# Kernel optimization log

Measured on AMD Instinct MI355X. Metric: run time of the kernel, lower is better.

## Reference

```python
import jax, jax.numpy as jnp
import numpy as np

B, S, H, NH = 2, 2048, 2048, 16
HD = H // NH


def setup_inputs() -> dict:
    key = jax.random.key(0)
    ks = jax.random.split(key, 10)
    s = 1.0 / np.sqrt(H)
    x = jax.random.normal(ks[0], (B, S, H), dtype=jnp.float32)
    # additive causal mask: 0 on/below diagonal, -1e9 above
    causal = jnp.tril(jnp.ones((S, S), dtype=bool))
    mask = jnp.where(causal, 0.0, -1e9).astype(jnp.float32)[None, None]
    return {
        "x": x,
        "mask": mask,
        "wq": jax.random.normal(ks[1], (H, H), jnp.float32) * s,
        "bq": jnp.zeros((H,), jnp.float32),
        "wk": jax.random.normal(ks[2], (H, H), jnp.float32) * s,
        "bk": jnp.zeros((H,), jnp.float32),
        "wv": jax.random.normal(ks[3], (H, H), jnp.float32) * s,
        "bv": jnp.zeros((H,), jnp.float32),
        "wo": jax.random.normal(ks[4], (H, H), jnp.float32) * s,
        "bo": jnp.zeros((H,), jnp.float32),
    }


def reference(x, mask, wq, bq, wk, bk, wv, bv, wo, bo):
    b, s, _ = x.shape
    scale = HD ** (-0.5)
    # projections -> [b, nh, s, hd]
    def split_heads(t):
        return t.reshape(b, s, NH, HD).transpose(0, 2, 1, 3)
    q = split_heads(x @ wq + bq)
    k = split_heads(x @ wk + bk)
    v = split_heads(x @ wv + bv)
    scores = jnp.einsum('bhqd,bhkd->bhqk', q, k) * scale + mask
    attn = jax.nn.softmax(scores, axis=-1)
    out = jnp.einsum('bhqk,bhkd->bhqd', attn, v)
    out = out.transpose(0, 2, 1, 3).reshape(b, s, H)
    return out @ wo + bo
```

## Files before the change

kernel.cpp:

```cpp
#include <hip/hip_runtime.h>


using bf16x8 = __attribute__((ext_vector_type(8))) short;
using bf16x4 = __attribute__((ext_vector_type(4))) short;
using f32x4  = __attribute__((ext_vector_type(4))) float;

#define S_LEN 2048
#define NHEAD 16
#define HDIM  128
#define HID   2048

__device__ __forceinline__ unsigned short f2bf(float f) {
    unsigned int u = __float_as_uint(f);
    u += 0x7fffu + ((u >> 16) & 1u);
    return (unsigned short)(u >> 16);
}
__device__ __forceinline__ void gl2lds16(const void* g, void* l) {
    __builtin_amdgcn_global_load_lds(
        (const __attribute__((address_space(1))) void*)g,
        (__attribute__((address_space(3))) void*)l, 16, 0, 0);
}

__device__ __forceinline__ f32x4 pv_mfma(bf16x4 a, bf16x4 b, f32x4 c) {
#if defined(__HIP_DEVICE_COMPILE__)
#if __has_builtin(__builtin_amdgcn_mfma_f32_16x16x16bf16_1k)
    return __builtin_amdgcn_mfma_f32_16x16x16bf16_1k(a, b, c, 0, 0, 0);
#else
    asm("v_mfma_f32_16x16x16_bf16 %0, %1, %2, %0" : "+v"(c) : "v"(a), "v"(b));
    return c;
#endif
#else
    (void)a; (void)b;
    return c;
#endif
}

__global__ void convert_x(const float* __restrict__ x, unsigned short* __restrict__ xb) {
    int i = (blockIdx.x * 256 + threadIdx.x) * 4;
    float4 v = *(const float4*)(x + i);
    ushort4 o;
    o.x = f2bf(v.x); o.y = f2bf(v.y); o.z = f2bf(v.z); o.w = f2bf(v.w);
    *(ushort4*)(xb + i) = o;
}

__global__ void convert_wt(const float* __restrict__ w0, const float* __restrict__ w1,
                           const float* __restrict__ w2, const float* __restrict__ w3,
                           unsigned short* __restrict__ t0, unsigned short* __restrict__ t1,
                           unsigned short* __restrict__ t2, unsigned short* __restrict__ t3) {
    __shared__ float tile[64][65];
    int z = blockIdx.z;
    const float* src = (z == 0) ? w0 : (z == 1) ? w1 : (z == 2) ? w2 : w3;
    unsigned short* dst = (z == 0) ? t0 : (z == 1) ? t1 : (z == 2) ? t2 : t3;
    int r0 = blockIdx.y * 64, c0 = blockIdx.x * 64;
    int t = threadIdx.x;
    for (int i = t; i < 64 * 64; i += 256) {
        int r = i >> 6, c = i & 63;
        tile[r][c] = src[(size_t)(r0 + r) * HID + c0 + c];
    }
    __syncthreads();
    for (int i = t; i < 64 * 64; i += 256) {
        int r = i & 63, c = i >> 6;
        dst[(size_t)(c0 + c) * HID + r0 + r] = f2bf(tile[r][c]);
    }
}

__device__ __forceinline__ void sched0() { __builtin_amdgcn_sched_barrier(0); }
__device__ __forceinline__ void w_lgkm4() { asm volatile("s_waitcnt lgkmcnt(4)" ::: "memory"); sched0(); }
__device__ __forceinline__ void w_lgkm0() { asm volatile("s_waitcnt lgkmcnt(0)" ::: "memory"); sched0(); }
template <int NJ> __device__ __forceinline__ void w_lgkm_4nj() {
    if constexpr (NJ == 3) { asm volatile("s_waitcnt lgkmcnt(7)" ::: "memory"); }
    else                   { asm volatile("s_waitcnt lgkmcnt(6)" ::: "memory"); }
    sched0();
}
template <int NJ> __device__ __forceinline__ void w_vm_ns() {
    if constexpr (NJ == 3) { asm volatile("s_waitcnt vmcnt(7)" ::: "memory"); }
    else                   { asm volatile("s_waitcnt vmcnt(6)" ::: "memory"); }
    sched0();
}
__device__ __forceinline__ void w_vm2() { asm volatile("s_waitcnt vmcnt(2)" ::: "memory"); sched0(); }
__device__ __forceinline__ void w_vm0() { asm volatile("s_waitcnt vmcnt(0)" ::: "memory"); sched0(); }
__device__ __forceinline__ void barx() {
    asm volatile("" ::: "memory");
    __builtin_amdgcn_s_barrier();
    asm volatile("" ::: "memory");
}

template <int MODE, int NJ>
__launch_bounds__(512, 2)
__global__ void gemmT(const unsigned short* __restrict__ A,
                      const unsigned short* __restrict__ Bt0,
                      const float* __restrict__ bias0,
                      const float* __restrict__ bias1,
                      const float* __restrict__ bias2,
                      unsigned short* __restrict__ C0,
                      unsigned short* __restrict__ C1,
                      unsigned short* __restrict__ C2,
                      float* __restrict__ Cf) {
    constexpr int BN = NJ * 64;
    __shared__ __align__(16) unsigned short lds[2 * 16384 + 2 * NJ * 4096];
    unsigned short* const A0 = lds;
    unsigned short* const A1 = lds + 16384;
    unsigned short* const B0 = lds + 32768;
    unsigned short* const B1 = lds + 32768 + NJ * 4096;

    const int CPX = (MODE == 1) ? 64 : 32;
    int vb = (blockIdx.x & 7) * CPX + (blockIdx.x >> 3);
    int m0  = (vb & 15) * 256;
    int n0g = (vb >> 4) * BN;

    int tid = threadIdx.x;
    int lane = tid & 63;
    int wv_ = tid >> 6;
    int wr = wv_ >> 2, wc = wv_ & 3;
    int l15 = lane & 15, quad = lane >> 4;

    int tr = tid >> 3;
    int tc = ((tid & 7) ^ (tr & 7)) << 3;
    const unsigned short* gA = A   + (size_t)(m0  + tr) * HID + tc;
    const unsigned short* gB = Bt0 + (size_t)(n0g + tr) * HID + tc;
    const int td8 = tid * 8;

    int arow0 = (wr * 128 + l15) * 64;
    int brow0 = (wc * (16 * NJ) + l15) * 64;
    int sw0 = ((quad ^ (l15 & 7)) << 3);
    int sw1 = (((4 + quad) ^ (l15 & 7)) << 3);

    f32x4 acc[8][NJ];
#pragma unroll
    for (int i = 0; i < 8; ++i)
#pragma unroll
        for (int j = 0; j < NJ; ++j) acc[i][j] = (f32x4){0.f, 0.f, 0.f, 0.f};

    bf16x8 aX[4], aY[4], b0v[NJ], b1v[NJ];

#define STAGE(kt, AD, BD) do { int _kc = (kt) * 64;                          \
    gl2lds16(gA + _kc,             (AD) + td8);                              \
    gl2lds16(gA + 64 * HID + _kc,  (AD) + 4096 + td8);                       \
    gl2lds16(gA + 128 * HID + _kc, (AD) + 8192 + td8);                       \
    gl2lds16(gA + 192 * HID + _kc, (AD) + 12288 + td8);                      \
    _Pragma("unroll")                                                        \
    for (int _r = 0; _r < NJ; ++_r)                                          \
        gl2lds16(gB + (size_t)(_r * 64) * HID + _kc, (BD) + _r * 4096 + td8); } while (0)

#define LDA4(dst, AD, QB, SW) do {                                           \
    dst[0] = *(const bf16x8*)((AD) + arow0 + ((QB) + 0) * 1024 + (SW));      \
    dst[1] = *(const bf16x8*)((AD) + arow0 + ((QB) + 1) * 1024 + (SW));      \
    dst[2] = *(const bf16x8*)((AD) + arow0 + ((QB) + 2) * 1024 + (SW));      \
    dst[3] = *(const bf16x8*)((AD) + arow0 + ((QB) + 3) * 1024 + (SW)); } while (0)

#define LDB(dst, BD, SW) do {                                                \
    _Pragma("unroll")                                                        \
    for (int _n = 0; _n < NJ; ++_n)                                          \
        dst[_n] = *(const bf16x8*)((BD) + brow0 + _n * 1024 + (SW)); } while (0)

#define MF(Q, a, b) do {                                                     \
    __builtin_amdgcn_s_setprio(1);                                           \
    _Pragma("unroll")                                                        \
    for (int mi = 0; mi < 4; ++mi)                                           \
        _Pragma("unroll")                                                    \
        for (int nj = 0; nj < NJ; ++nj)                                      \
            acc[(Q) * 4 + mi][nj] =                                          \
                __builtin_amdgcn_mfma_f32_16x16x32_bf16(a[mi], b[nj],        \
                                                        acc[(Q) * 4 + mi][nj], 0, 0, 0); \
    __builtin_amdgcn_s_setprio(0); } while (0)

#define TILE(AD, BD, AN, BN_, ks) do {                                       \
    LDA4(aY, AD, 4, sw0);                                      \
    w_lgkm4();                                   \
    MF(0, aX, b0v);                                                          \
    LDA4(aX, AD, 0, sw1);                                                    \
    LDB(b1v, BD, sw1);                                   \
    w_lgkm_4nj<NJ>();                                          \
    MF(1, aY, b0v);                                                          \
    LDA4(aY, AD, 4, sw1);                                      \
    w_lgkm4();                                             \
    MF(0, aX, b1v);                                                          \
    w_lgkm0();                                \
    barx();                              \
    STAGE(ks, AD, BD);                          \
    w_vm_ns<NJ>();                        \
    barx();                                  \
    LDA4(aX, AN, 0, sw0);                                                    \
    LDB(b0v, BN_, sw0);                   \
    sched0();                                                                \
    MF(1, aY, b1v);                          \
} while (0)

    STAGE(0, A0, B0);
    STAGE(1, A1, B1);
    w_vm_ns<NJ>();
    barx();
    LDA4(aX, A0, 0, sw0);
    LDB(b0v, B0, sw0);

    for (int t = 0; t < 32; t += 2) {
        TILE(A0, B0, A1, B1, (t + 2 < 32) ? t + 2 : 31);
        TILE(A1, B1, A0, B0, (t + 3 < 32) ? t + 3 : 31);
    }
    asm volatile("s_waitcnt vmcnt(0) lgkmcnt(0)" ::: "memory");

#undef TILE
#undef STAGE
#undef LDA4
#undef LDB
#undef MF

#pragma unroll
    for (int j = 0; j < NJ; ++j) {
        int n = n0g + wc * (16 * NJ) + j * 16 + l15;
        int zj = (MODE == 1) ? (n >> 11) : 0;
        int nn = (MODE == 1) ? (n & 2047) : n;
        float bn = (MODE == 1)
                     ? ((zj == 0) ? bias0[nn] : (zj == 1) ? bias1[nn] : bias2[nn])
                     : bias0[nn];
        unsigned short* Cz = (zj == 0) ? C0 : (zj == 1) ? C1 : C2;
#pragma unroll
        for (int i = 0; i < 8; ++i) {
            int mb = m0 + wr * 128 + i * 16 + quad * 4;
            if (MODE == 1 && zj == 2) {
                int b = mb >> 11, s = mb & 2047, h = nn >> 7, d = nn & 127;
                int kt = s >> 4, qv = (s >> 2) & 3, ct = d >> 4, lv = d & 15;
                size_t addr = ((((size_t)((b << 4) + h) * 128 + kt) * 4 + (ct >> 1)) * 4 + qv) * 128
                              + lv * 8 + (ct & 1) * 4;
                ushort4 o;
                o.x = f2bf(acc[i][j][0] + bn);
                o.y = f2bf(acc[i][j][1] + bn);
                o.z = f2bf(acc[i][j][2] + bn);
                o.w = f2bf(acc[i][j][3] + bn);
                *(ushort4*)&Cz[addr] = o;
            } else {
#pragma unroll
                for (int reg = 0; reg < 4; ++reg) {
                    int m = mb + reg;
                    float v = acc[i][j][reg] + bn;
                    if (MODE == 0) {
                        Cf[(size_t)m * HID + nn] = v;
                    } else {
                        int b = m >> 11, s = m & 2047, h = nn >> 7, d = nn & 127;
                        if (zj == 1) {
                            int kt = s >> 4, lk = s & 15, kk = d >> 5, qk = (d >> 3) & 3, e = d & 7;
                            size_t addr = ((((size_t)((b << 4) + h) * 128 + kt) * 4 + kk) * 4 + qk) * 128
                                          + lk * 8 + e;
                            Cz[addr] = f2bf(v);
                        } else {
                            Cz[(size_t)(((b << 4) + h) * S_LEN + s) * HDIM + d] = f2bf(v);
                        }
                    }
                }
            }
        }
    }
}

__launch_bounds__(256, 2)
__global__ void attn_kernel(const unsigned short* __restrict__ Qg,
                            const unsigned short* __restrict__ Kp,
                            const unsigned short* __restrict__ Vp,
                            unsigned short* __restrict__ O) {
    __shared__ __align__(16) unsigned short kv[2][4096];

    int linear = blockIdx.x;
    int xcd = linear & 7;
    int u = linear >> 3;
    int bh = xcd * 4 + (u & 3);
    int q = u >> 2;
    int b = bh >> 4, h = bh & 15;

    int tid = threadIdx.x, lane = tid & 63, w = tid >> 6;
    int l15 = lane & 15, quad = lane >> 4;

    const unsigned short* Qb = Qg + (size_t)bh * (S_LEN * HDIM);
    const unsigned short* Kg = Kp + (size_t)bh * 262144;
    const unsigned short* Vg = Vp + (size_t)bh * 262144;
    const float k2 = 0.08838834764831845f * 1.4426950408889634f;

    const int frag = quad * 128 + l15 * 8;
    const int td8 = tid * 8;

#define VLO(x) __builtin_shufflevector(x, x, 0, 1, 2, 3)
#define VHI(x) __builtin_shufflevector(x, x, 4, 5, 6, 7)
#define ASTAGE(kt, bf) do { size_t _g = (size_t)(kt) * 2048 + td8;             \
    gl2lds16(Kg + _g, &kv[bf][td8]);                                           \
    gl2lds16(Vg + _g, &kv[bf][2048 + td8]); } while (0)

    auto run_qblock = [&](int qb) {
        int s  = 4 * qb + w;
        int r0 = s * 16;
        int N  = 4 * qb + 4;

        bf16x8 qf[4];
#pragma unroll
        for (int kk = 0; kk < 4; ++kk)
            qf[kk] = *(const bf16x8*)&Qb[(size_t)(r0 + l15) * HDIM + kk * 32 + quad * 8];

        f32x4 o_acc[8];
#pragma unroll
        for (int c = 0; c < 8; ++c) o_acc[c] = (f32x4){0.f, 0.f, 0.f, 0.f};
        float l_part = 0.f;

        ASTAGE(0, 0);
        for (int kt = 0; kt < N; ++kt) {
            int nk = (kt + 1 < N) ? kt + 1 : kt;
            ASTAGE(nk, (kt + 1) & 1);
            w_vm2();
            barx();

            const unsigned short* KL = &kv[kt & 1][frag];
            const unsigned short* VL = &kv[kt & 1][2048 + frag];
            bf16x8 kb0 = *(const bf16x8*)(KL);
            bf16x8 kb1 = *(const bf16x8*)(KL + 512);
            bf16x8 kb2 = *(const bf16x8*)(KL + 1024);
            bf16x8 kb3 = *(const bf16x8*)(KL + 1536);
            bf16x8 v0 = *(const bf16x8*)(VL);
            bf16x8 v1 = *(const bf16x8*)(VL + 512);
            bf16x8 v2 = *(const bf16x8*)(VL + 1024);
            bf16x8 v3 = *(const bf16x8*)(VL + 1536);

            f32x4 st0 = (f32x4){0.f, 0.f, 0.f, 0.f};
            f32x4 st1 = (f32x4){0.f, 0.f, 0.f, 0.f};
            __builtin_amdgcn_s_setprio(1);
            st0 = __builtin_amdgcn_mfma_f32_16x16x32_bf16(kb0, qf[0], st0, 0, 0, 0);
            st1 = __builtin_amdgcn_mfma_f32_16x16x32_bf16(kb1, qf[1], st1, 0, 0, 0);
            st0 = __builtin_amdgcn_mfma_f32_16x16x32_bf16(kb2, qf[2], st0, 0, 0, 0);
            st1 = __builtin_amdgcn_mfma_f32_16x16x32_bf16(kb3, qf[3], st1, 0, 0, 0);
            __builtin_amdgcn_s_setprio(0);
            f32x4 stv = st0 + st1;

            float p0, p1, p2, p3;
            int doff = kt - s;
            if (doff >= 0) {
                int d16 = doff << 4;
                p0 = (d16 + quad * 4 + 0 <= l15) ? exp2f(stv[0] * k2) : 0.f;
                p1 = (d16 + quad * 4 + 1 <= l15) ? exp2f(stv[1] * k2) : 0.f;
                p2 = (d16 + quad * 4 + 2 <= l15) ? exp2f(stv[2] * k2) : 0.f;
                p3 = (d16 + quad * 4 + 3 <= l15) ? exp2f(stv[3] * k2) : 0.f;
            } else {
                p0 = exp2f(stv[0] * k2); p1 = exp2f(stv[1] * k2);
                p2 = exp2f(stv[2] * k2); p3 = exp2f(stv[3] * k2);
            }
            l_part += (p0 + p1) + (p2 + p3);

            bf16x4 pf;
            pf[0] = (short)f2bf(p0); pf[1] = (short)f2bf(p1);
            pf[2] = (short)f2bf(p2); pf[3] = (short)f2bf(p3);

            __builtin_amdgcn_s_setprio(1);
            o_acc[0] = pv_mfma(pf, VLO(v0), o_acc[0]);
            o_acc[1] = pv_mfma(pf, VHI(v0), o_acc[1]);
            o_acc[2] = pv_mfma(pf, VLO(v1), o_acc[2]);
            o_acc[3] = pv_mfma(pf, VHI(v1), o_acc[3]);
            o_acc[4] = pv_mfma(pf, VLO(v2), o_acc[4]);
            o_acc[5] = pv_mfma(pf, VHI(v2), o_acc[5]);
            o_acc[6] = pv_mfma(pf, VLO(v3), o_acc[6]);
            o_acc[7] = pv_mfma(pf, VHI(v3), o_acc[7]);
            __builtin_amdgcn_s_setprio(0);
            barx();
        }
        w_vm0();
        barx();

        float lp = l_part;
        lp += __shfl_xor(lp, 16, 64);
        lp += __shfl_xor(lp, 32, 64);
#pragma unroll
        for (int reg = 0; reg < 4; ++reg) {
            float l = __shfl(lp, quad * 4 + reg, 64);
            float inv = 1.f / l;
            int srow = r0 + quad * 4 + reg;
            unsigned short* op = O + (size_t)(b * S_LEN + srow) * HID + h * HDIM;
#pragma unroll
            for (int ct = 0; ct < 8; ++ct)
                op[ct * 16 + l15] = f2bf(o_acc[ct][reg] * inv);
        }
    };

    run_qblock(q);
    run_qblock(31 - q);

#undef ASTAGE
#undef VLO
#undef VHI
}

extern "C" void kernel_launch(void* const* d_in, const int* in_sizes, int n_in,
                              void* d_out, int out_size, void* d_ws, size_t ws_size,
                              hipStream_t stream) {
    (void)in_sizes; (void)n_in; (void)out_size; (void)ws_size;
    const float* x  = (const float*)d_in[0];
    const float* wq = (const float*)d_in[2];
    const float* bq = (const float*)d_in[3];
    const float* wk = (const float*)d_in[4];
    const float* bk = (const float*)d_in[5];
    const float* wv = (const float*)d_in[6];
    const float* bv = (const float*)d_in[7];
    const float* wo = (const float*)d_in[8];
    const float* bo = (const float*)d_in[9];
    float* out = (float*)d_out;

    unsigned short* ws = (unsigned short*)d_ws;
    const size_t WSZ = 4194304;
    unsigned short* wqT = ws;
    unsigned short* wkT = ws + WSZ;
    unsigned short* wvT = ws + 2 * WSZ;
    unsigned short* woT = ws + 3 * WSZ;
    unsigned short* xb  = ws + 4 * WSZ;
    unsigned short* Ab  = ws + 4 * WSZ;
    unsigned short* Qb  = ws + 6 * WSZ;
    unsigned short* Kb  = ws + 8 * WSZ;
    unsigned short* Vb  = ws + 10 * WSZ;

    convert_x<<<dim3(8192), 256, 0, stream>>>(x, xb);
    convert_wt<<<dim3(32, 32, 4), 256, 0, stream>>>(wq, wk, wv, wo, wqT, wkT, wvT, woT);
    gemmT<1, 3><<<dim3(512), 512, 0, stream>>>(xb, wqT, bq, bk, bv,
                                               Qb, Kb, Vb, nullptr);
    attn_kernel<<<dim3(512), 256, 0, stream>>>(Qb, Kb, Vb, Ab);
    gemmT<0, 2><<<dim3(256), 512, 0, stream>>>(Ab, woT, bo, nullptr, nullptr,
                                               nullptr, nullptr, nullptr, out);
}
```

Baseline: 394.7 us.

## Shrink GEMM tiles to 128x128 for higher occupancy and merge convert kernels

Moves the projection GEMMs from 256xNJ*64 tiles with 8x NJ accumulators per wave to 128x128 tiles with 4x2 accumulators. Launch bounds rise to 4 blocks per CU and the grids grow to 1536 and 512 blocks, aiming to fill the GPU better and hide latency through occupancy. The pipelined K-loop is simplified to one MFMA batch per half-tile with retuned waitcnts. The x and weight conversion kernels are fused into a single launch to save one launch. Smaller tiles lower data reuse per block and raise global and LDS traffic.

Measured after the change: 407.1 us. 1.03x slower.

```diff
diff --git a/kernel.cpp b/kernel.cpp
--- a/kernel.cpp
+++ b/kernel.cpp
@@ -35,20 +35,23 @@
 #endif
 }
 
-__global__ void convert_x(const float* __restrict__ x, unsigned short* __restrict__ xb) {
-    int i = (blockIdx.x * 256 + threadIdx.x) * 4;
-    float4 v = *(const float4*)(x + i);
-    ushort4 o;
-    o.x = f2bf(v.x); o.y = f2bf(v.y); o.z = f2bf(v.z); o.w = f2bf(v.w);
-    *(ushort4*)(xb + i) = o;
-}
-
-__global__ void convert_wt(const float* __restrict__ w0, const float* __restrict__ w1,
-                           const float* __restrict__ w2, const float* __restrict__ w3,
-                           unsigned short* __restrict__ t0, unsigned short* __restrict__ t1,
-                           unsigned short* __restrict__ t2, unsigned short* __restrict__ t3) {
+__global__ void convert_all(const float* __restrict__ x,
+                            const float* __restrict__ w0, const float* __restrict__ w1,
+                            const float* __restrict__ w2, const float* __restrict__ w3,
+                            unsigned short* __restrict__ xb,
+                            unsigned short* __restrict__ t0, unsigned short* __restrict__ t1,
+                            unsigned short* __restrict__ t2, unsigned short* __restrict__ t3) {
+    int z = blockIdx.z;
+    if (z >= 4) {
+        int lin = (z - 4) * 1024 + blockIdx.y * 32 + blockIdx.x;
+        int i = (lin * 256 + threadIdx.x) * 4;
+        float4 v = *(const float4*)(x + i);
+        ushort4 o;
+        o.x = f2bf(v.x); o.y = f2bf(v.y); o.z = f2bf(v.z); o.w = f2bf(v.w);
+        *(ushort4*)(xb + i) = o;
+        return;
+    }
     __shared__ float tile[64][65];
-    int z = blockIdx.z;
     const float* src = (z == 0) ? w0 : (z == 1) ? w1 : (z == 2) ? w2 : w3;
     unsigned short* dst = (z == 0) ? t0 : (z == 1) ? t1 : (z == 2) ? t2 : t3;
     int r0 = blockIdx.y * 64, c0 = blockIdx.x * 64;
@@ -65,28 +68,19 @@
 }
 
 __device__ __forceinline__ void sched0() { __builtin_amdgcn_sched_barrier(0); }
-__device__ __forceinline__ void w_lgkm4() { asm volatile("s_waitcnt lgkmcnt(4)" ::: "memory"); sched0(); }
+__device__ __forceinline__ void w_lgkm6() { asm volatile("s_waitcnt lgkmcnt(6)" ::: "memory"); sched0(); }
 __device__ __forceinline__ void w_lgkm0() { asm volatile("s_waitcnt lgkmcnt(0)" ::: "memory"); sched0(); }
-template <int NJ> __device__ __forceinline__ void w_lgkm_4nj() {
-    if constexpr (NJ == 3) { asm volatile("s_waitcnt lgkmcnt(7)" ::: "memory"); }
-    else                   { asm volatile("s_waitcnt lgkmcnt(6)" ::: "memory"); }
-    sched0();
-}
-template <int NJ> __device__ __forceinline__ void w_vm_ns() {
-    if constexpr (NJ == 3) { asm volatile("s_waitcnt vmcnt(7)" ::: "memory"); }
-    else                   { asm volatile("s_waitcnt vmcnt(6)" ::: "memory"); }
-    sched0();
-}
-__device__ __forceinline__ void w_vm2() { asm volatile("s_waitcnt vmcnt(2)" ::: "memory"); sched0(); }
-__device__ __forceinline__ void w_vm0() { asm volatile("s_waitcnt vmcnt(0)" ::: "memory"); sched0(); }
+__device__ __forceinline__ void w_vm4()   { asm volatile("s_waitcnt vmcnt(4)" ::: "memory");   sched0(); }
+__device__ __forceinline__ void w_vm2()   { asm volatile("s_waitcnt vmcnt(2)" ::: "memory");   sched0(); }
+__device__ __forceinline__ void w_vm0()   { asm volatile("s_waitcnt vmcnt(0)" ::: "memory");   sched0(); }
 __device__ __forceinline__ void barx() {
     asm volatile("" ::: "memory");
     __builtin_amdgcn_s_barrier();
     asm volatile("" ::: "memory");
 }
 
-template <int MODE, int NJ>
-__launch_bounds__(512, 2)
+template <int MODE>
+__launch_bounds__(512, 4)
 __global__ void gemmT(const unsigned short* __restrict__ A,
                       const unsigned short* __restrict__ Bt0,
                       const float* __restrict__ bias0,
@@ -96,17 +90,18 @@
                       unsigned short* __restrict__ C1,
                       unsigned short* __restrict__ C2,
                       float* __restrict__ Cf) {
-    constexpr int BN = NJ * 64;
-    __shared__ __align__(16) unsigned short lds[2 * 16384 + 2 * NJ * 4096];
+    __shared__ __align__(16) unsigned short lds[32768];
     unsigned short* const A0 = lds;
-    unsigned short* const A1 = lds + 16384;
-    unsigned short* const B0 = lds + 32768;
-    unsigned short* const B1 = lds + 32768 + NJ * 4096;
-
-    const int CPX = (MODE == 1) ? 64 : 32;
+    unsigned short* const A1 = lds + 8192;
+    unsigned short* const B0 = lds + 16384;
+    unsigned short* const B1 = lds + 24576;
+
+    const int NT = (MODE == 1) ? 48 : 16;
+    const int CPX = (MODE == 1) ? 192 : 64;
     int vb = (blockIdx.x & 7) * CPX + (blockIdx.x >> 3);
-    int m0  = (vb & 15) * 256;
-    int n0g = (vb >> 4) * BN;
+    int m0  = (vb & 31) * 128;
+    int n0g = (vb >> 5) * 128;
+    (void)NT;
 
     int tid = threadIdx.x;
     int lane = tid & 63;
@@ -120,78 +115,67 @@
     const unsigned short* gB = Bt0 + (size_t)(n0g + tr) * HID + tc;
     const int td8 = tid * 8;
 
-    int arow0 = (wr * 128 + l15) * 64;
-    int brow0 = (wc * (16 * NJ) + l15) * 64;
+    int arow0 = (wr * 64 + l15) * 64;
+    int brow0 = (wc * 32 + l15) * 64;
     int sw0 = ((quad ^ (l15 & 7)) << 3);
     int sw1 = (((4 + quad) ^ (l15 & 7)) << 3);
 
-    f32x4 acc[8][NJ];
-#pragma unroll
-    for (int i = 0; i < 8; ++i)
-#pragma unroll
-        for (int j = 0; j < NJ; ++j) acc[i][j] = (f32x4){0.f, 0.f, 0.f, 0.f};
-
-    bf16x8 aX[4], aY[4], b0v[NJ], b1v[NJ];
+    f32x4 acc[4][2];
+#pragma unroll
+    for (int i = 0; i < 4; ++i)
+#pragma unroll
+        for (int j = 0; j < 2; ++j) acc[i][j] = (f32x4){0.f, 0.f, 0.f, 0.f};
+
+    bf16x8 aX[4], aY[4], b0v[2], b1v[2];
 
 #define STAGE(kt, AD, BD) do { int _kc = (kt) * 64;                          \
-    gl2lds16(gA + _kc,             (AD) + td8);                              \
-    gl2lds16(gA + 64 * HID + _kc,  (AD) + 4096 + td8);                       \
-    gl2lds16(gA + 128 * HID + _kc, (AD) + 8192 + td8);                       \
-    gl2lds16(gA + 192 * HID + _kc, (AD) + 12288 + td8);                      \
-    _Pragma("unroll")                                                        \
-    for (int _r = 0; _r < NJ; ++_r)                                          \
-        gl2lds16(gB + (size_t)(_r * 64) * HID + _kc, (BD) + _r * 4096 + td8); } while (0)
-
-#define LDA4(dst, AD, QB, SW) do {                                           \
-    dst[0] = *(const bf16x8*)((AD) + arow0 + ((QB) + 0) * 1024 + (SW));      \
-    dst[1] = *(const bf16x8*)((AD) + arow0 + ((QB) + 1) * 1024 + (SW));      \
-    dst[2] = *(const bf16x8*)((AD) + arow0 + ((QB) + 2) * 1024 + (SW));      \
-    dst[3] = *(const bf16x8*)((AD) + arow0 + ((QB) + 3) * 1024 + (SW)); } while (0)
-
-#define LDB(dst, BD, SW) do {                                                \
-    _Pragma("unroll")                                                        \
-    for (int _n = 0; _n < NJ; ++_n)                                          \
-        dst[_n] = *(const bf16x8*)((BD) + brow0 + _n * 1024 + (SW)); } while (0)
-
-#define MF(Q, a, b) do {                                                     \
+    gl2lds16(gA + _kc,            (AD) + td8);                               \
+    gl2lds16(gA + 64 * HID + _kc, (AD) + 4096 + td8);                        \
+    gl2lds16(gB + _kc,            (BD) + td8);                               \
+    gl2lds16(gB + 64 * HID + _kc, (BD) + 4096 + td8); } while (0)
+
+#define LDA4(dst, AD, SW) do {                                               \
+    dst[0] = *(const bf16x8*)((AD) + arow0 + 0 * 1024 + (SW));               \
+    dst[1] = *(const bf16x8*)((AD) + arow0 + 1 * 1024 + (SW));               \
+    dst[2] = *(const bf16x8*)((AD) + arow0 + 2 * 1024 + (SW));               \
+    dst[3] = *(const bf16x8*)((AD) + arow0 + 3 * 1024 + (SW)); } while (0)
+
+#define LDB2(dst, BD, SW) do {                                               \
+    dst[0] = *(const bf16x8*)((BD) + brow0 + 0 * 1024 + (SW));               \
+    dst[1] = *(const bf16x8*)((BD) + brow0 + 1 * 1024 + (SW)); } while (0)
+
+#define MF(a, b) do {                                                        \
     __builtin_amdgcn_s_setprio(1);                                           \
     _Pragma("unroll")                                                        \
     for (int mi = 0; mi < 4; ++mi)                                           \
         _Pragma("unroll")                                                    \
-        for (int nj = 0; nj < NJ; ++nj)                                      \
-            acc[(Q) * 4 + mi][nj] =                                          \
+        for (int nj = 0; nj < 2; ++nj)                                       \
+            acc[mi][nj] =                                                    \
                 __builtin_amdgcn_mfma_f32_16x16x32_bf16(a[mi], b[nj],        \
-                                                        acc[(Q) * 4 + mi][nj], 0, 0, 0); \
+                                                        acc[mi][nj], 0, 0, 0); \
     __builtin_amdgcn_s_setprio(0); } while (0)
 
 #define TILE(AD, BD, AN, BN_, ks) do {                                       \
-    LDA4(aY, AD, 4, sw0);                                      \
-    w_lgkm4();                                   \
-    MF(0, aX, b0v);                                                          \
-    LDA4(aX, AD, 0, sw1);                                                    \
-    LDB(b1v, BD, sw1);                                   \
-    w_lgkm_4nj<NJ>();                                          \
-    MF(1, aY, b0v);                                                          \
-    LDA4(aY, AD, 4, sw1);                                      \
-    w_lgkm4();                                             \
-    MF(0, aX, b1v);                                                          \
+    LDA4(aY, AD, sw1); LDB2(b1v, BD, sw1);               \
+    w_lgkm6();                                \
+    w_vm4();                         \
+    MF(aX, b0v);                              \
     w_lgkm0();                                \
     barx();                              \
-    STAGE(ks, AD, BD);                          \
-    w_vm_ns<NJ>();                        \
-    barx();                                  \
-    LDA4(aX, AN, 0, sw0);                                                    \
-    LDB(b0v, BN_, sw0);                   \
+    STAGE(ks, AD, BD);                         \
+    w_vm4();                         \
+    barx();                                     \
+    LDA4(aX, AN, sw0); LDB2(b0v, BN_, sw0);     \
     sched0();                                                                \
-    MF(1, aY, b1v);                          \
+    MF(aY, b1v);                        \
 } while (0)
 
     STAGE(0, A0, B0);
     STAGE(1, A1, B1);
-    w_vm_ns<NJ>();
+    w_vm4();
     barx();
-    LDA4(aX, A0, 0, sw0);
-    LDB(b0v, B0, sw0);
+    LDA4(aX, A0, sw0);
+    LDB2(b0v, B0, sw0);
 
     for (int t = 0; t < 32; t += 2) {
         TILE(A0, B0, A1, B1, (t + 2 < 32) ? t + 2 : 31);
@@ -202,12 +186,12 @@
 #undef TILE
 #undef STAGE
 #undef LDA4
-#undef LDB
+#undef LDB2
 #undef MF
 
 #pragma unroll
-    for (int j = 0; j < NJ; ++j) {
-        int n = n0g + wc * (16 * NJ) + j * 16 + l15;
+    for (int j = 0; j < 2; ++j) {
+        int n = n0g + wc * 32 + j * 16 + l15;
         int zj = (MODE == 1) ? (n >> 11) : 0;
         int nn = (MODE == 1) ? (n & 2047) : n;
         float bn = (MODE == 1)
@@ -215,8 +199,8 @@
                      : bias0[nn];
         unsigned short* Cz = (zj == 0) ? C0 : (zj == 1) ? C1 : C2;
 #pragma unroll
-        for (int i = 0; i < 8; ++i) {
-            int mb = m0 + wr * 128 + i * 16 + quad * 4;
+        for (int i = 0; i < 4; ++i) {
+            int mb = m0 + wr * 64 + i * 16 + quad * 4;
             if (MODE == 1 && zj == 2) {
                 int b = mb >> 11, s = mb & 2047, h = nn >> 7, d = nn & 127;
                 int kt = s >> 4, qv = (s >> 2) & 3, ct = d >> 4, lv = d & 15;
@@ -409,11 +393,11 @@
     unsigned short* Kb  = ws + 8 * WSZ;
     unsigned short* Vb  = ws + 10 * WSZ;
 
-    convert_x<<<dim3(8192), 256, 0, stream>>>(x, xb);
-    convert_wt<<<dim3(32, 32, 4), 256, 0, stream>>>(wq, wk, wv, wo, wqT, wkT, wvT, woT);
-    gemmT<1, 3><<<dim3(512), 512, 0, stream>>>(xb, wqT, bq, bk, bv,
-                                               Qb, Kb, Vb, nullptr);
+    convert_all<<<dim3(32, 32, 12), 256, 0, stream>>>(x, wq, wk, wv, wo,
+                                                      xb, wqT, wkT, wvT, woT);
+    gemmT<1><<<dim3(1536), 512, 0, stream>>>(xb, wqT, bq, bk, bv,
+                                             Qb, Kb, Vb, nullptr);
     attn_kernel<<<dim3(512), 256, 0, stream>>>(Qb, Kb, Vb, Ab);
-    gemmT<0, 2><<<dim3(256), 512, 0, stream>>>(Ab, woT, bo, nullptr, nullptr,
-                                               nullptr, nullptr, nullptr, out);
-}
+    gemmT<0><<<dim3(512), 512, 0, stream>>>(Ab, woT, bo, nullptr, nullptr,
+                                            nullptr, nullptr, nullptr, out);
+}
```

## Split attention into one q-block per CTA with two-tile staging; merge convert kernels

Applied to the files above, without the earlier changes.

The attention kernel now launches 1024 blocks, each handling a single 64-row query block, where before each of 512 blocks processed a paired q and 31-q. The KV stage is doubled to two 16-key tiles per buffer (32 KB LDS) with the wait count adjusted to match, and occupancy is raised to 4 blocks per SM. Blocks are ordered largest-first so long causal blocks start early and load balance comes from the scheduler instead of explicit pairing. Separately, the x conversion and the weight transpose/convert are fused into one launch to save a kernel launch. The risks are uneven per-block work and more LDS pressure from the larger buffers.

After: 410.7 us. 4.0% more time.

```diff
diff --git a/kernel.cpp b/kernel.cpp
--- a/kernel.cpp
+++ b/kernel.cpp
@@ -35,20 +35,23 @@
 #endif
 }
 
-__global__ void convert_x(const float* __restrict__ x, unsigned short* __restrict__ xb) {
-    int i = (blockIdx.x * 256 + threadIdx.x) * 4;
-    float4 v = *(const float4*)(x + i);
-    ushort4 o;
-    o.x = f2bf(v.x); o.y = f2bf(v.y); o.z = f2bf(v.z); o.w = f2bf(v.w);
-    *(ushort4*)(xb + i) = o;
-}
-
-__global__ void convert_wt(const float* __restrict__ w0, const float* __restrict__ w1,
-                           const float* __restrict__ w2, const float* __restrict__ w3,
-                           unsigned short* __restrict__ t0, unsigned short* __restrict__ t1,
-                           unsigned short* __restrict__ t2, unsigned short* __restrict__ t3) {
+__global__ void convert_all(const float* __restrict__ x,
+                            const float* __restrict__ w0, const float* __restrict__ w1,
+                            const float* __restrict__ w2, const float* __restrict__ w3,
+                            unsigned short* __restrict__ xb,
+                            unsigned short* __restrict__ t0, unsigned short* __restrict__ t1,
+                            unsigned short* __restrict__ t2, unsigned short* __restrict__ t3) {
+    int z = blockIdx.z;
+    if (z >= 4) {
+        int lin = (z - 4) * 1024 + blockIdx.y * 32 + blockIdx.x;
+        int i = (lin * 256 + threadIdx.x) * 4;
+        float4 v = *(const float4*)(x + i);
+        ushort4 o;
+        o.x = f2bf(v.x); o.y = f2bf(v.y); o.z = f2bf(v.z); o.w = f2bf(v.w);
+        *(ushort4*)(xb + i) = o;
+        return;
+    }
     __shared__ float tile[64][65];
-    int z = blockIdx.z;
     const float* src = (z == 0) ? w0 : (z == 1) ? w1 : (z == 2) ? w2 : w3;
     unsigned short* dst = (z == 0) ? t0 : (z == 1) ? t1 : (z == 2) ? t2 : t3;
     int r0 = blockIdx.y * 64, c0 = blockIdx.x * 64;
@@ -77,7 +80,7 @@
     else                   { asm volatile("s_waitcnt vmcnt(6)" ::: "memory"); }
     sched0();
 }
-__device__ __forceinline__ void w_vm2() { asm volatile("s_waitcnt vmcnt(2)" ::: "memory"); sched0(); }
+__device__ __forceinline__ void w_vm4() { asm volatile("s_waitcnt vmcnt(4)" ::: "memory"); sched0(); }
 __device__ __forceinline__ void w_vm0() { asm volatile("s_waitcnt vmcnt(0)" ::: "memory"); sched0(); }
 __device__ __forceinline__ void barx() {
     asm volatile("" ::: "memory");
@@ -252,22 +255,26 @@
     }
 }
 
-__launch_bounds__(256, 2)
+__launch_bounds__(256, 4)
 __global__ void attn_kernel(const unsigned short* __restrict__ Qg,
                             const unsigned short* __restrict__ Kp,
                             const unsigned short* __restrict__ Vp,
                             unsigned short* __restrict__ O) {
-    __shared__ __align__(16) unsigned short kv[2][4096];
+    __shared__ __align__(16) unsigned short kv[2][8192];
 
     int linear = blockIdx.x;
     int xcd = linear & 7;
     int u = linear >> 3;
-    int bh = xcd * 4 + (u & 3);
-    int q = u >> 2;
+    int bh = xcd * 4 + (u >> 5);
+    int q = 31 - (u & 31);
     int b = bh >> 4, h = bh & 15;
 
     int tid = threadIdx.x, lane = tid & 63, w = tid >> 6;
     int l15 = lane & 15, quad = lane >> 4;
+
+    int s  = 4 * q + w;
+    int r0 = s * 16;
+    int NC = 2 * q + 2;
 
     const unsigned short* Qb = Qg + (size_t)bh * (S_LEN * HDIM);
     const unsigned short* Kg = Kp + (size_t)bh * 262144;
@@ -279,105 +286,100 @@
 
 #define VLO(x) __builtin_shufflevector(x, x, 0, 1, 2, 3)
 #define VHI(x) __builtin_shufflevector(x, x, 4, 5, 6, 7)
-#define ASTAGE(kt, bf) do { size_t _g = (size_t)(kt) * 2048 + td8;             \
-    gl2lds16(Kg + _g, &kv[bf][td8]);                                           \
-    gl2lds16(Vg + _g, &kv[bf][2048 + td8]); } while (0)
-
-    auto run_qblock = [&](int qb) {
-        int s  = 4 * qb + w;
-        int r0 = s * 16;
-        int N  = 4 * qb + 4;
-
-        bf16x8 qf[4];
-#pragma unroll
-        for (int kk = 0; kk < 4; ++kk)
-            qf[kk] = *(const bf16x8*)&Qb[(size_t)(r0 + l15) * HDIM + kk * 32 + quad * 8];
-
-        f32x4 o_acc[8];
-#pragma unroll
-        for (int c = 0; c < 8; ++c) o_acc[c] = (f32x4){0.f, 0.f, 0.f, 0.f};
-        float l_part = 0.f;
-
-        ASTAGE(0, 0);
-        for (int kt = 0; kt < N; ++kt) {
-            int nk = (kt + 1 < N) ? kt + 1 : kt;
-            ASTAGE(nk, (kt + 1) & 1);
-            w_vm2();
-            barx();
-
-            const unsigned short* KL = &kv[kt & 1][frag];
-            const unsigned short* VL = &kv[kt & 1][2048 + frag];
-            bf16x8 kb0 = *(const bf16x8*)(KL);
-            bf16x8 kb1 = *(const bf16x8*)(KL + 512);
-            bf16x8 kb2 = *(const bf16x8*)(KL + 1024);
-            bf16x8 kb3 = *(const bf16x8*)(KL + 1536);
-            bf16x8 v0 = *(const bf16x8*)(VL);
-            bf16x8 v1 = *(const bf16x8*)(VL + 512);
-            bf16x8 v2 = *(const bf16x8*)(VL + 1024);
-            bf16x8 v3 = *(const bf16x8*)(VL + 1536);
-
-            f32x4 st0 = (f32x4){0.f, 0.f, 0.f, 0.f};
-            f32x4 st1 = (f32x4){0.f, 0.f, 0.f, 0.f};
-            __builtin_amdgcn_s_setprio(1);
-            st0 = __builtin_amdgcn_mfma_f32_16x16x32_bf16(kb0, qf[0], st0, 0, 0, 0);
-            st1 = __builtin_amdgcn_mfma_f32_16x16x32_bf16(kb1, qf[1], st1, 0, 0, 0);
-            st0 = __builtin_amdgcn_mfma_f32_16x16x32_bf16(kb2, qf[2], st0, 0, 0, 0);
-            st1 = __builtin_amdgcn_mfma_f32_16x16x32_bf16(kb3, qf[3], st1, 0, 0, 0);
-            __builtin_amdgcn_s_setprio(0);
-            f32x4 stv = st0 + st1;
-
-            float p0, p1, p2, p3;
-            int doff = kt - s;
-            if (doff >= 0) {
-                int d16 = doff << 4;
-                p0 = (d16 + quad * 4 + 0 <= l15) ? exp2f(stv[0] * k2) : 0.f;
-                p1 = (d16 + quad * 4 + 1 <= l15) ? exp2f(stv[1] * k2) : 0.f;
-                p2 = (d16 + quad * 4 + 2 <= l15) ? exp2f(stv[2] * k2) : 0.f;
-                p3 = (d16 + quad * 4 + 3 <= l15) ? exp2f(stv[3] * k2) : 0.f;
-            } else {
-                p0 = exp2f(stv[0] * k2); p1 = exp2f(stv[1] * k2);
-                p2 = exp2f(stv[2] * k2); p3 = exp2f(stv[3] * k2);
-            }
-            l_part += (p0 + p1) + (p2 + p3);
-
-            bf16x4 pf;
-            pf[0] = (short)f2bf(p0); pf[1] = (short)f2bf(p1);
-            pf[2] = (short)f2bf(p2); pf[3] = (short)f2bf(p3);
-
-            __builtin_amdgcn_s_setprio(1);
-            o_acc[0] = pv_mfma(pf, VLO(v0), o_acc[0]);
-            o_acc[1] = pv_mfma(pf, VHI(v0), o_acc[1]);
-            o_acc[2] = pv_mfma(pf, VLO(v1), o_acc[2]);
-            o_acc[3] = pv_mfma(pf, VHI(v1), o_acc[3]);
-            o_acc[4] = pv_mfma(pf, VLO(v2), o_acc[4]);
-            o_acc[5] = pv_mfma(pf, VHI(v2), o_acc[5]);
-            o_acc[6] = pv_mfma(pf, VLO(v3), o_acc[6]);
-            o_acc[7] = pv_mfma(pf, VHI(v3), o_acc[7]);
-            __builtin_amdgcn_s_setprio(0);
-            barx();
-        }
-        w_vm0();
+#define ASTAGE2(c, bf) do {                                                    \
+    size_t _g0 = (size_t)(2 * (c)) * 2048 + td8;                               \
+    size_t _g1 = (size_t)(2 * (c) + 1) * 2048 + td8;                           \
+    gl2lds16(Kg + _g0, &kv[bf][td8]);                                          \
+    gl2lds16(Vg + _g0, &kv[bf][2048 + td8]);                                   \
+    gl2lds16(Kg + _g1, &kv[bf][4096 + td8]);                                   \
+    gl2lds16(Vg + _g1, &kv[bf][6144 + td8]); } while (0)
+
+    bf16x8 qf[4];
+#pragma unroll
+    for (int kk = 0; kk < 4; ++kk)
+        qf[kk] = *(const bf16x8*)&Qb[(size_t)(r0 + l15) * HDIM + kk * 32 + quad * 8];
+
+    f32x4 o_acc[8];
+#pragma unroll
+    for (int c = 0; c < 8; ++c) o_acc[c] = (f32x4){0.f, 0.f, 0.f, 0.f};
+    float l_part = 0.f;
+
+#define COMP(kt, bf, half) do {                                                \
+    const unsigned short* KL = &kv[bf][(half) * 4096 + frag];                  \
+    const unsigned short* VL = KL + 2048;                                      \
+    bf16x8 kb0 = *(const bf16x8*)(KL);                                         \
+    bf16x8 kb1 = *(const bf16x8*)(KL + 512);                                   \
+    bf16x8 kb2 = *(const bf16x8*)(KL + 1024);                                  \
+    bf16x8 kb3 = *(const bf16x8*)(KL + 1536);                                  \
+    bf16x8 v0 = *(const bf16x8*)(VL);                                          \
+    bf16x8 v1 = *(const bf16x8*)(VL + 512);                                    \
+    bf16x8 v2 = *(const bf16x8*)(VL + 1024);                                   \
+    bf16x8 v3 = *(const bf16x8*)(VL + 1536);                                   \
+    f32x4 st0 = (f32x4){0.f, 0.f, 0.f, 0.f};                                   \
+    f32x4 st1 = (f32x4){0.f, 0.f, 0.f, 0.f};                                   \
+    __builtin_amdgcn_s_setprio(1);                                             \
+    st0 = __builtin_amdgcn_mfma_f32_16x16x32_bf16(kb0, qf[0], st0, 0, 0, 0);   \
+    st1 = __builtin_amdgcn_mfma_f32_16x16x32_bf16(kb1, qf[1], st1, 0, 0, 0);   \
+    st0 = __builtin_amdgcn_mfma_f32_16x16x32_bf16(kb2, qf[2], st0, 0, 0, 0);   \
+    st1 = __builtin_amdgcn_mfma_f32_16x16x32_bf16(kb3, qf[3], st1, 0, 0, 0);   \
+    __builtin_amdgcn_s_setprio(0);                                             \
+    f32x4 stv = st0 + st1;                                                     \
+    float p0, p1, p2, p3;                                                      \
+    int doff = (kt) - s;                                                       \
+    if (doff >= 0) {                                                           \
+        int d16 = doff << 4;                                                   \
+        p0 = (d16 + quad * 4 + 0 <= l15) ? exp2f(stv[0] * k2) : 0.f;           \
+        p1 = (d16 + quad * 4 + 1 <= l15) ? exp2f(stv[1] * k2) : 0.f;           \
+        p2 = (d16 + quad * 4 + 2 <= l15) ? exp2f(stv[2] * k2) : 0.f;           \
+        p3 = (d16 + quad * 4 + 3 <= l15) ? exp2f(stv[3] * k2) : 0.f;           \
+    } else {                                                                   \
+        p0 = exp2f(stv[0] * k2); p1 = exp2f(stv[1] * k2);                      \
+        p2 = exp2f(stv[2] * k2); p3 = exp2f(stv[3] * k2);                      \
+    }                                                                          \
+    l_part += (p0 + p1) + (p2 + p3);                                           \
+    bf16x4 pf;                                                                 \
+    pf[0] = (short)f2bf(p0); pf[1] = (short)f2bf(p1);                          \
+    pf[2] = (short)f2bf(p2); pf[3] = (short)f2bf(p3);                          \
+    __builtin_amdgcn_s_setprio(1);                                             \
+    o_acc[0] = pv_mfma(pf, VLO(v0), o_acc[0]);                                 \
+    o_acc[1] = pv_mfma(pf, VHI(v0), o_acc[1]);                                 \
+    o_acc[2] = pv_mfma(pf, VLO(v1), o_acc[2]);                                 \
+    o_acc[3] = pv_mfma(pf, VHI(v1), o_acc[3]);                                 \
+    o_acc[4] = pv_mfma(pf, VLO(v2), o_acc[4]);                                 \
+    o_acc[5] = pv_mfma(pf, VHI(v2), o_acc[5]);                                 \
+    o_acc[6] = pv_mfma(pf, VLO(v3), o_acc[6]);                                 \
+    o_acc[7] = pv_mfma(pf, VHI(v3), o_acc[7]);                                 \
+    __builtin_amdgcn_s_setprio(0);                                             \
+} while (0)
+
+    ASTAGE2(0, 0);
+    for (int c = 0; c < NC; ++c) {
+        int nc2 = (c + 1 < NC) ? c + 1 : c;
+        ASTAGE2(nc2, (c + 1) & 1);
+        w_vm4();
         barx();
-
-        float lp = l_part;
-        lp += __shfl_xor(lp, 16, 64);
-        lp += __shfl_xor(lp, 32, 64);
-#pragma unroll
-        for (int reg = 0; reg < 4; ++reg) {
-            float l = __shfl(lp, quad * 4 + reg, 64);
-            float inv = 1.f / l;
-            int srow = r0 + quad * 4 + reg;
-            unsigned short* op = O + (size_t)(b * S_LEN + srow) * HID + h * HDIM;
-#pragma unroll
-            for (int ct = 0; ct < 8; ++ct)
-                op[ct * 16 + l15] = f2bf(o_acc[ct][reg] * inv);
-        }
-    };
-
-    run_qblock(q);
-    run_qblock(31 - q);
-
-#undef ASTAGE
+        COMP(2 * c,     (c & 1), 0);
+        COMP(2 * c + 1, (c & 1), 1);
+        barx();
+    }
+    w_vm0();
+
+    float lp = l_part;
+    lp += __shfl_xor(lp, 16, 64);
+    lp += __shfl_xor(lp, 32, 64);
+#pragma unroll
+    for (int reg = 0; reg < 4; ++reg) {
+        float l = __shfl(lp, quad * 4 + reg, 64);
+        float inv = 1.f / l;
+        int srow = r0 + quad * 4 + reg;
+        unsigned short* op = O + (size_t)(b * S_LEN + srow) * HID + h * HDIM;
+#pragma unroll
+        for (int ct = 0; ct < 8; ++ct)
+            op[ct * 16 + l15] = f2bf(o_acc[ct][reg] * inv);
+    }
+
+#undef COMP
+#undef ASTAGE2
 #undef VLO
 #undef VHI
 }
@@ -409,11 +411,11 @@
     unsigned short* Kb  = ws + 8 * WSZ;
     unsigned short* Vb  = ws + 10 * WSZ;
 
-    convert_x<<<dim3(8192), 256, 0, stream>>>(x, xb);
-    convert_wt<<<dim3(32, 32, 4), 256, 0, stream>>>(wq, wk, wv, wo, wqT, wkT, wvT, woT);
+    convert_all<<<dim3(32, 32, 12), 256, 0, stream>>>(x, wq, wk, wv, wo,
+                                                      xb, wqT, wkT, wvT, woT);
     gemmT<1, 3><<<dim3(512), 512, 0, stream>>>(xb, wqT, bq, bk, bv,
                                                Qb, Kb, Vb, nullptr);
-    attn_kernel<<<dim3(512), 256, 0, stream>>>(Qb, Kb, Vb, Ab);
+    attn_kernel<<<dim3(1024), 256, 0, stream>>>(Qb, Kb, Vb, Ab);
     gemmT<0, 2><<<dim3(256), 512, 0, stream>>>(Ab, woT, bo, nullptr, nullptr,
                                                nullptr, nullptr, nullptr, out);
 }
```
